# Optimization experiments

Measured on AMD Instinct MI355X. Metric: run time of the kernel, lower is better.

Reference implementation:

```python
import jax, jax.numpy as jnp
import numpy as np

EPS_DIST = 1e-7  # matches torch: log((d+1)/(d+1e-7))


def _cdist(x, p):
    # x: (B, N, D), p: (P, D) -> (B, N, P) Euclidean distances
    x2 = jnp.sum(x * x, axis=-1, keepdims=True)        # (B, N, 1)
    p2 = jnp.sum(p * p, axis=-1)                       # (P,)
    d2 = x2 + p2[None, None, :] - 2.0 * jnp.einsum('bnd,pd->bnp', x, p)
    return jnp.sqrt(jnp.maximum(d2, 1e-12))


def setup_inputs() -> dict:
    key = jax.random.key(0)
    k1, k2, k3 = jax.random.split(key, 3)
    B, C, H, W = 32, 2048, 14, 14
    num_classes, npc = 200, 10
    P = num_classes * npc
    x = jax.random.normal(k1, (B, C, H, W), dtype=jnp.float32)
    prototypes = jax.random.normal(k2, (1, P, C), dtype=jnp.float32)
    fc_w = jax.random.normal(k3, (num_classes, P), dtype=jnp.float32) * 0.02
    return {"x": x, "prototypes": prototypes, "fc_w": fc_w}


def reference(x, prototypes, fc_w):
    B, C, H, W = x.shape
    feats = x.reshape(B, C, H * W).transpose(0, 2, 1)   # (B, HW, D)
    protos = prototypes[0]                              # (P, D)
    num_classes = fc_w.shape[0]
    npc = protos.shape[0] // num_classes

    distances = _cdist(feats, protos)                   # (B, HW, P)
    similarity = jnp.log((distances + 1.0) / (distances + EPS_DIST))
    max_similarity = jnp.max(similarity, axis=1)        # (B, P)
    min_distances = jnp.min(distances, axis=1)          # (B, P)
    min_distances_per_class = min_distances.reshape(B, num_classes, npc)
    scores = max_similarity @ fc_w.T                    # (B, num_classes)
    return scores, min_distances_per_class
```

## Files before the change

### kernel.cpp

```cpp
#include <hip/hip_runtime.h>

#define INF_BITS 0x7F800000u
#define AS1 __attribute__((address_space(1)))
#define AS3 __attribute__((address_space(3)))

typedef float f32x4 __attribute__((ext_vector_type(4)));
typedef int i32x4 __attribute__((ext_vector_type(4)));
typedef int i32x8 __attribute__((ext_vector_type(8)));
typedef unsigned int u32x2 __attribute__((ext_vector_type(2)));
typedef unsigned int u32x4 __attribute__((ext_vector_type(4)));

template <int SEL>
static __device__ __forceinline__ float dq8(unsigned int w) {
  return __builtin_amdgcn_cvt_f32_fp8((int)w, SEL);
}

__global__ __launch_bounds__(256) void k_prep_p(const float* __restrict__ protos,
                                                unsigned char* __restrict__ pTf,
                                                float* __restrict__ p2,
                                                unsigned int* __restrict__ outu) {
  const int row = blockIdx.x;
  const int tid = threadIdx.x;
  const int gi = row * 256 + tid;
  if (gi < 64000) outu[6400 + gi] = INF_BITS;
  __shared__ float red[4];
  float s = 0.f;
  unsigned int w0 = 0u, w1 = 0u;
  if (row < 2000) {
    const float* src = protos + (size_t)row * 2048 + tid * 8;
    f32x4 a = *(const f32x4*)src;
    f32x4 c = *(const f32x4*)(src + 4);
    w0 = (unsigned int)__builtin_amdgcn_cvt_pk_fp8_f32(a.x, a.y, 0, false);
    w0 = (unsigned int)__builtin_amdgcn_cvt_pk_fp8_f32(a.z, a.w, (int)w0, true);
    w1 = (unsigned int)__builtin_amdgcn_cvt_pk_fp8_f32(c.x, c.y, 0, false);
    w1 = (unsigned int)__builtin_amdgcn_cvt_pk_fp8_f32(c.z, c.w, (int)w1, true);
    float q;
    q = dq8<0>(w0); s += q * q;
    q = dq8<1>(w0); s += q * q;
    q = dq8<2>(w0); s += q * q;
    q = dq8<3>(w0); s += q * q;
    q = dq8<0>(w1); s += q * q;
    q = dq8<1>(w1); s += q * q;
    q = dq8<2>(w1); s += q * q;
    q = dq8<3>(w1); s += q * q;
  }
  *(u32x2*)(pTf + (size_t)row * 2048 + tid * 8) = (u32x2){w0, w1};
  #pragma unroll
  for (int off = 32; off; off >>= 1) s += __shfl_xor(s, off);
  if ((tid & 63) == 0) red[tid >> 6] = s;
  __syncthreads();
  if (tid == 0) p2[row] = red[0] + red[1] + red[2] + red[3];
}

__global__ __launch_bounds__(256) void k_prep_x(const float* __restrict__ x,
                                                unsigned char* __restrict__ xTf,
                                                float* __restrict__ x2p,
                                                float* __restrict__ x2) {
  const int kt = blockIdx.x;
  const int b  = blockIdx.y;
  const int tid = threadIdx.x;
  if (b == 32) {
    u32x4* pad = (u32x4*)(xTf + (size_t)6272 * 2048);
    #pragma unroll
    for (int j = tid; j < 512; j += 256)
      pad[kt * 512 + j] = (u32x4){0u, 0u, 0u, 0u};
    if (kt == 0 && tid < 128) x2[6272 + tid] = __uint_as_float(INF_BITS);
    return;
  }
  __shared__ unsigned char Ls[64][208];
  const float* src = x + ((size_t)b * 2048 + (size_t)kt * 64) * 196;
  for (int idx = tid; idx < 3136; idx += 256) {
    const int kk = idx / 49, c4 = idx - kk * 49;
    f32x4 v = *(const f32x4*)(src + (size_t)kk * 196 + c4 * 4);
    unsigned int w = (unsigned int)__builtin_amdgcn_cvt_pk_fp8_f32(v.x, v.y, 0, false);
    w = (unsigned int)__builtin_amdgcn_cvt_pk_fp8_f32(v.z, v.w, (int)w, true);
    *(unsigned int*)&Ls[kk][c4 * 4] = w;
  }
  __syncthreads();
  if (tid < 196) {
    float s = 0.f;
    #pragma unroll
    for (int j = 0; j < 64; ++j) {
      float v = dq8<0>((unsigned int)Ls[j][tid]);
      s += v * v;
    }
    x2p[kt * 6272 + b * 196 + tid] = s;
  }
  unsigned char* dstb = xTf + (size_t)b * 196 * 2048 + kt * 64;
  for (int idx = tid; idx < 784; idx += 256) {
    const int n = idx >> 2, q = idx & 3;
    const int k0 = q * 16;
    u32x4 v;
    #pragma unroll
    for (int j = 0; j < 4; ++j) {
      v[j] = (unsigned int)Ls[k0 + 4 * j + 0][n] |
             ((unsigned int)Ls[k0 + 4 * j + 1][n] << 8) |
             ((unsigned int)Ls[k0 + 4 * j + 2][n] << 16) |
             ((unsigned int)Ls[k0 + 4 * j + 3][n] << 24);
    }
    *(u32x4*)(dstb + (size_t)n * 2048 + k0) = v;
  }
}

__global__ void k_x2r(const float* __restrict__ x2p, float* __restrict__ x2) {
  int i = blockIdx.x * blockDim.x + threadIdx.x;
  if (i >= 6272) return;
  float s = 0.f;
  #pragma unroll
  for (int c = 0; c < 32; ++c) s += x2p[c * 6272 + i];
  x2[i] = s;
}

__global__ __launch_bounds__(512, 2) void k_main(
    const unsigned char* __restrict__ pTf, const unsigned char* __restrict__ xTf,
    const float* __restrict__ p2, const float* __restrict__ x2,
    unsigned int* __restrict__ outu) {
  const int orig = blockIdx.x;
  const int wgid = (orig & 7) * 25 + (orig >> 3);
  const int ptpair = wgid / 50;
  const int rem = wgid - ptpair * 50;
  const int ptile = ptpair * 2 + (rem & 1);
  const int mtile = rem >> 1;
  const int p0 = ptile * 256;
  const int m0 = mtile * 256;
  const int tid = threadIdx.x;
  const int lane = tid & 63;
  const int w = tid >> 6;
  const int wp = w >> 2;
  const int wn = w & 3;
  const int lr = lane & 15;
  const int lg = lane >> 4;

  __shared__ __align__(16) char S[131072];

  f32x4 acc[8][4];
  #pragma unroll
  for (int mi = 0; mi < 8; ++mi)
    #pragma unroll
    for (int ni = 0; ni < 4; ++ni)
      acc[mi][ni] = (f32x4){0.f, 0.f, 0.f, 0.f};

  const int rowbase = tid >> 3;
  const int chunk = (tid & 7) ^ (rowbase & 7);
  const char* gA = (const char*)pTf + (size_t)(p0 + rowbase) * 2048 + chunk * 16;
  const char* gB = (const char*)xTf + (size_t)(m0 + rowbase) * 2048 + chunk * 16;
  const int wbase = w * 1024;

#define STAGE_A(c_, kt_, h_) do {                                              \
    const char* s_ = gA + (size_t)((h_) * 128 * 2048) + (size_t)(kt_) * 128;   \
    _Pragma("unroll")                                                          \
    for (int j_ = 0; j_ < 2; ++j_)                                             \
      __builtin_amdgcn_global_load_lds(                                        \
          (const AS1 void*)(s_ + (size_t)j_ * 64 * 2048),                      \
          (AS3 void*)(S + (c_) * 32768 + (h_) * 16384 + j_ * 8192 + wbase),    \
          16, 0, 0);                                                           \
  } while (0)
#define STAGE_B(c_, kt_, h_) do {                                              \
    const char* s_ = gB + (size_t)((h_) * 128 * 2048) + (size_t)(kt_) * 128;   \
    _Pragma("unroll")                                                          \
    for (int j_ = 0; j_ < 2; ++j_)                                             \
      __builtin_amdgcn_global_load_lds(                                        \
          (const AS1 void*)(s_ + (size_t)j_ * 64 * 2048),                      \
          (AS3 void*)(S + 65536 + (c_) * 32768 + (h_) * 16384 + j_ * 8192 + wbase), \
          16, 0, 0);                                                           \
  } while (0)

  const int swz = ((lr & 7) << 4);
  const int koffA = (lg * 32) ^ swz;
  const int arow = (wp * 128 + lr) * 128;
  const int brow = (wn * 64 + lr) * 128;

#define READ_A4(dst_, c_, hf_)                                                 \
    _Pragma("unroll")                                                          \
    for (int mi_ = 0; mi_ < 4; ++mi_) {                                        \
      const char* p_ = S + (c_) * 32768 + arow + ((hf_) * 4 + mi_) * 2048;     \
      u32x4 lo_ = *(const u32x4*)(p_ + koffA);                                 \
      u32x4 hi_ = *(const u32x4*)(p_ + (koffA ^ 16));                          \
      dst_[mi_] = __builtin_bit_cast(i32x8,                                    \
          __builtin_shufflevector(lo_, hi_, 0, 1, 2, 3, 4, 5, 6, 7));          \
    }
#define READ_B4(dst_, c_)                                                      \
    _Pragma("unroll")                                                          \
    for (int ni_ = 0; ni_ < 4; ++ni_) {                                        \
      const char* p_ = S + 65536 + (c_) * 32768 + brow + ni_ * 2048;           \
      u32x4 lo_ = *(const u32x4*)(p_ + koffA);                                 \
      u32x4 hi_ = *(const u32x4*)(p_ + (koffA ^ 16));                          \
      dst_[ni_] = __builtin_bit_cast(i32x8,                                    \
          __builtin_shufflevector(lo_, hi_, 0, 1, 2, 3, 4, 5, 6, 7));          \
    }

#define PH_BAR() do { __builtin_amdgcn_sched_barrier(0);                       \
    __builtin_amdgcn_s_barrier(); __builtin_amdgcn_sched_barrier(0); } while (0)
#define LGKM0() do { asm volatile("s_waitcnt lgkmcnt(0)" ::: "memory");        \
    __builtin_amdgcn_sched_barrier(0); } while (0)
#define MFMA_Q(mlo_, af_, bf_) do { __builtin_amdgcn_s_setprio(1);             \
    _Pragma("unroll")                                                          \
    for (int mi_ = 0; mi_ < 4; ++mi_)                                          \
      _Pragma("unroll")                                                        \
      for (int ni_ = 0; ni_ < 4; ++ni_)                                        \
        acc[(mlo_) + mi_][ni_] =                                               \
            __builtin_amdgcn_mfma_scale_f32_16x16x128_f8f6f4(                  \
                af_[mi_], bf_[ni_], acc[(mlo_) + mi_][ni_],                    \
                0, 0, 0, 0x7F7F7F7F, 0, 0x7F7F7F7F);                           \
    __builtin_amdgcn_s_setprio(0); } while (0)

#define KT_BODY(kt_, c_, sa_, sb_, vm_) do {                                   \
    i32x8 af[4], bf[4];                                                        \
    READ_B4(bf, c_);                                                           \
    READ_A4(af, c_, 0);                                                        \
    if (sa_) { STAGE_A((c_) ^ 1, (kt_) + 1, 0); STAGE_A((c_) ^ 1, (kt_) + 1, 1); } \
    PH_BAR(); LGKM0();                                                         \
    MFMA_Q(0, af, bf);                                                         \
    PH_BAR();                                                                  \
    READ_A4(af, c_, 1);                                                        \
    if (sb_) { STAGE_B(c_, (kt_) + 2, 0); STAGE_B(c_, (kt_) + 2, 1); }         \
    PH_BAR(); LGKM0();                                                         \
    MFMA_Q(4, af, bf);                                                         \
    if ((vm_) == 4)      asm volatile("s_waitcnt vmcnt(4)" ::: "memory");      \
    else if ((vm_) == 0) asm volatile("s_waitcnt vmcnt(0)" ::: "memory");      \
    __builtin_amdgcn_sched_barrier(0);                                         \
    PH_BAR();                                                                  \
  } while (0)

  STAGE_A(0, 0, 0); STAGE_A(0, 0, 1);
  STAGE_B(0, 0, 0); STAGE_B(0, 0, 1);
  STAGE_B(1, 1, 0); STAGE_B(1, 1, 1);
  asm volatile("s_waitcnt vmcnt(4)" ::: "memory");
  __builtin_amdgcn_sched_barrier(0);
  __builtin_amdgcn_s_barrier();
  __builtin_amdgcn_sched_barrier(0);

  #pragma unroll 1
  for (int it = 0; it < 7; ++it) {
    KT_BODY(2 * it, 0, 1, 1, 4);
    KT_BODY(2 * it + 1, 1, 1, 1, 4);
  }
  KT_BODY(14, 0, 1, 0, 0);
  KT_BODY(15, 1, 0, 0, -1);
#undef KT_BODY
#undef MFMA_Q
#undef READ_A4
#undef READ_B4
#undef STAGE_A
#undef STAGE_B

  const int wm_base = m0 + wn * 64;
  const int b_lo = wm_base / 196;
  int b_hi = (wm_base + 63) / 196;
  if (b_hi > 31) b_hi = 31;
  const bool wave_ok = (b_lo < 32);
  float x2v[4];
  int seg0[4];
  #pragma unroll
  for (int ni = 0; ni < 4; ++ni) {
    const int m = wm_base + ni * 16 + lr;
    x2v[ni] = x2[m];
    seg0[ni] = ((m / 196) == b_lo);
  }
  const float INF = __uint_as_float(INF_BITS);
  #pragma unroll
  for (int mi = 0; mi < 8; ++mi) {
    const int prow = p0 + wp * 128 + mi * 16 + 4 * lg;
    #pragma unroll
    for (int j = 0; j < 4; ++j) {
      const int p = prow + j;
      const float pp = p2[p];
      float ma = INF, mb = INF;
      #pragma unroll
      for (int ni = 0; ni < 4; ++ni) {
        const float d2 = x2v[ni] + pp - 2.f * acc[mi][ni][j];
        ma = fminf(ma, seg0[ni] ? d2 : INF);
        mb = fminf(mb, seg0[ni] ? INF : d2);
      }
      #pragma unroll
      for (int off = 1; off < 16; off <<= 1) {
        ma = fminf(ma, __shfl_xor(ma, off));
        mb = fminf(mb, __shfl_xor(mb, off));
      }
      if (lr == 0 && p < 2000 && wave_ok) {
        atomicMin(&outu[6400 + b_lo * 2000 + p], __float_as_uint(fmaxf(ma, 0.f)));
        if (b_hi != b_lo)
          atomicMin(&outu[6400 + b_hi * 2000 + p], __float_as_uint(fmaxf(mb, 0.f)));
      }
    }
  }
}

__global__ void k_post(float* __restrict__ out, float* __restrict__ simbuf) {
  int i = blockIdx.x * blockDim.x + threadIdx.x;
  if (i >= 64000) return;
  float d2 = out[6400 + i];
  float d = sqrtf(fmaxf(d2, 1e-12f));
  out[6400 + i] = d;
  simbuf[i] = logf((d + 1.0f) / (d + 1e-7f));
}

__global__ __launch_bounds__(256) void k_scores(const float* __restrict__ fc_w,
                                                const float* __restrict__ simbuf,
                                                float* __restrict__ out) {
  const int id = blockIdx.x * 4 + (threadIdx.x >> 6);
  const int lane = threadIdx.x & 63;
  const int b = id / 200;
  const int c = id - b * 200;
  const f32x4* sv = (const f32x4*)(simbuf + (size_t)b * 2000);
  const f32x4* wv = (const f32x4*)(fc_w + (size_t)c * 2000);
  float s = 0.f;
  #pragma unroll
  for (int it = 0; it < 8; ++it) {
    int i = lane + it * 64;
    if (i < 500) {
      f32x4 a = sv[i], w4 = wv[i];
      s += a.x * w4.x + a.y * w4.y + a.z * w4.z + a.w * w4.w;
    }
  }
  #pragma unroll
  for (int off = 32; off; off >>= 1) s += __shfl_xor(s, off);
  if (lane == 0) out[b * 200 + c] = s;
}

extern "C" void kernel_launch(void* const* d_in, const int* in_sizes, int n_in,
                              void* d_out, int out_size, void* d_ws, size_t ws_size,
                              hipStream_t stream) {
  const float* x      = (const float*)d_in[0];
  const float* protos = (const float*)d_in[1];
  const float* fc_w   = (const float*)d_in[2];
  float* out = (float*)d_out;

  char* wsb = (char*)d_ws;
  unsigned char* pTf = (unsigned char*)wsb;
  unsigned char* xTf = (unsigned char*)(wsb + 4194304);
  float* p2   = (float*)(wsb + 17301504);
  float* x2   = (float*)(wsb + 17309696);
  float* x2p  = (float*)(wsb + 17335296);
  float* simb = (float*)(wsb + 17335296);

  k_prep_p<<<2048, 256, 0, stream>>>(protos, pTf, p2, (unsigned int*)d_out);
  k_prep_x<<<dim3(32, 33), 256, 0, stream>>>(x, xTf, x2p, x2);
  k_x2r<<<25, 256, 0, stream>>>(x2p, x2);
  k_main<<<200, 512, 0, stream>>>(pTf, xTf, p2, x2, (unsigned int*)d_out);
  k_post<<<250, 256, 0, stream>>>(out, simb);
  k_scores<<<1600, 256, 0, stream>>>(fc_w, simb, out);
}
```

Baseline: 87.52 us.

## Interleave per-row A fragment LDS reads with MFMAs and cut barriers per k-step

The inner k-step no longer reads four A fragments, waits, runs sixteen MFMAs and repeats. It now streams one A row fragment at a time, double-buffered in two registers, so each LDS read overlaps the MFMAs of the previous row. The A prefetch is issued at the top of the step, and the B prefetch and vmcnt wait move after all MFMAs, leaving two barriers per step instead of four. This should hide LDS latency and reduce synchronisation stalls, but it relies on the compiler leaving the reads and MFMAs in that order and on the LDS buffer reuse staying race-free. The final step skips the trailing barriers.

```diff
diff --git a/kernel.cpp b/kernel.cpp
--- a/kernel.cpp
+++ b/kernel.cpp
@@ -170,15 +170,13 @@
   const int arow = (wp * 128 + lr) * 128;
   const int brow = (wn * 64 + lr) * 128;
 
-#define READ_A4(dst_, c_, hf_)                                                 \
-    _Pragma("unroll")                                                          \
-    for (int mi_ = 0; mi_ < 4; ++mi_) {                                        \
-      const char* p_ = S + (c_) * 32768 + arow + ((hf_) * 4 + mi_) * 2048;     \
-      u32x4 lo_ = *(const u32x4*)(p_ + koffA);                                 \
-      u32x4 hi_ = *(const u32x4*)(p_ + (koffA ^ 16));                          \
-      dst_[mi_] = __builtin_bit_cast(i32x8,                                    \
-          __builtin_shufflevector(lo_, hi_, 0, 1, 2, 3, 4, 5, 6, 7));          \
-    }
+#define READ_A1(dst_, c_, a_) do {                                             \
+    const char* p_ = S + (c_) * 32768 + arow + (a_) * 2048;                    \
+    u32x4 lo_ = *(const u32x4*)(p_ + koffA);                                   \
+    u32x4 hi_ = *(const u32x4*)(p_ + (koffA ^ 16));                            \
+    dst_ = __builtin_bit_cast(i32x8,                                           \
+        __builtin_shufflevector(lo_, hi_, 0, 1, 2, 3, 4, 5, 6, 7));            \
+  } while (0)
 #define READ_B4(dst_, c_)                                                      \
     _Pragma("unroll")                                                          \
     for (int ni_ = 0; ni_ < 4; ++ni_) {                                        \
@@ -189,57 +187,58 @@
           __builtin_shufflevector(lo_, hi_, 0, 1, 2, 3, 4, 5, 6, 7));          \
     }
 
-#define PH_BAR() do { __builtin_amdgcn_sched_barrier(0);                       \
-    __builtin_amdgcn_s_barrier(); __builtin_amdgcn_sched_barrier(0); } while (0)
-#define LGKM0() do { asm volatile("s_waitcnt lgkmcnt(0)" ::: "memory");        \
-    __builtin_amdgcn_sched_barrier(0); } while (0)
-#define MFMA_Q(mlo_, af_, bf_) do { __builtin_amdgcn_s_setprio(1);             \
+#define SCHED() __builtin_amdgcn_sched_barrier(0)
+#define SBAR() do { SCHED(); __builtin_amdgcn_s_barrier(); SCHED(); } while (0)
+#define LGKM0() do { asm volatile("s_waitcnt lgkmcnt(0)" ::: "memory"); SCHED(); } while (0)
+#define MFMA4(mi_, af_, bf_) do { __builtin_amdgcn_s_setprio(1);               \
     _Pragma("unroll")                                                          \
-    for (int mi_ = 0; mi_ < 4; ++mi_)                                          \
-      _Pragma("unroll")                                                        \
-      for (int ni_ = 0; ni_ < 4; ++ni_)                                        \
-        acc[(mlo_) + mi_][ni_] =                                               \
-            __builtin_amdgcn_mfma_scale_f32_16x16x128_f8f6f4(                  \
-                af_[mi_], bf_[ni_], acc[(mlo_) + mi_][ni_],                    \
-                0, 0, 0, 0x7F7F7F7F, 0, 0x7F7F7F7F);                           \
+    for (int ni_ = 0; ni_ < 4; ++ni_)                                          \
+      acc[mi_][ni_] = __builtin_amdgcn_mfma_scale_f32_16x16x128_f8f6f4(        \
+          af_, bf_[ni_], acc[mi_][ni_], 0, 0, 0, 0x7F7F7F7F, 0, 0x7F7F7F7F);   \
     __builtin_amdgcn_s_setprio(0); } while (0)
 
-#define KT_BODY(kt_, c_, sa_, sb_, vm_) do {                                   \
-    i32x8 af[4], bf[4];                                                        \
+#define KT_BODY(kt_, c_, sa_, sb_, vm_, tail_) do {                            \
+    if (sa_) { STAGE_A((c_) ^ 1, (kt_) + 1, 0); STAGE_A((c_) ^ 1, (kt_) + 1, 1); } \
+    i32x8 bf[4], af0, af1;                                                     \
     READ_B4(bf, c_);                                                           \
-    READ_A4(af, c_, 0);                                                        \
-    if (sa_) { STAGE_A((c_) ^ 1, (kt_) + 1, 0); STAGE_A((c_) ^ 1, (kt_) + 1, 1); } \
-    PH_BAR(); LGKM0();                                                         \
-    MFMA_Q(0, af, bf);                                                         \
-    PH_BAR();                                                                  \
-    READ_A4(af, c_, 1);                                                        \
-    if (sb_) { STAGE_B(c_, (kt_) + 2, 0); STAGE_B(c_, (kt_) + 2, 1); }         \
-    PH_BAR(); LGKM0();                                                         \
-    MFMA_Q(4, af, bf);                                                         \
-    if ((vm_) == 4)      asm volatile("s_waitcnt vmcnt(4)" ::: "memory");      \
-    else if ((vm_) == 0) asm volatile("s_waitcnt vmcnt(0)" ::: "memory");      \
-    __builtin_amdgcn_sched_barrier(0);                                         \
-    PH_BAR();                                                                  \
+    READ_A1(af0, c_, 0);                                                       \
+    READ_A1(af1, c_, 1); MFMA4(0, af0, bf); SCHED();                           \
+    READ_A1(af0, c_, 2); MFMA4(1, af1, bf); SCHED();                           \
+    READ_A1(af1, c_, 3); MFMA4(2, af0, bf); SCHED();                           \
+    READ_A1(af0, c_, 4); MFMA4(3, af1, bf); SCHED();                           \
+    READ_A1(af1, c_, 5); MFMA4(4, af0, bf); SCHED();                           \
+    READ_A1(af0, c_, 6); MFMA4(5, af1, bf); SCHED();                           \
+    READ_A1(af1, c_, 7); MFMA4(6, af0, bf); SCHED();                           \
+    MFMA4(7, af1, bf);                                                         \
+    if (!(tail_)) {                                                            \
+      LGKM0();                                                                 \
+      SBAR();                                               \
+      if (sb_) { STAGE_B(c_, (kt_) + 2, 0); STAGE_B(c_, (kt_) + 2, 1); }       \
+      if ((vm_) == 4)      asm volatile("s_waitcnt vmcnt(4)" ::: "memory");    \
+      else if ((vm_) == 0) asm volatile("s_waitcnt vmcnt(0)" ::: "memory");    \
+      SCHED();                                                                 \
+      SBAR();                                             \
+    }                                                                          \
   } while (0)
 
   STAGE_A(0, 0, 0); STAGE_A(0, 0, 1);
   STAGE_B(0, 0, 0); STAGE_B(0, 0, 1);
   STAGE_B(1, 1, 0); STAGE_B(1, 1, 1);
   asm volatile("s_waitcnt vmcnt(4)" ::: "memory");
-  __builtin_amdgcn_sched_barrier(0);
+  SCHED();
   __builtin_amdgcn_s_barrier();
-  __builtin_amdgcn_sched_barrier(0);
+  SCHED();
 
   #pragma unroll 1
   for (int it = 0; it < 7; ++it) {
-    KT_BODY(2 * it, 0, 1, 1, 4);
-    KT_BODY(2 * it + 1, 1, 1, 1, 4);
-  }
-  KT_BODY(14, 0, 1, 0, 0);
-  KT_BODY(15, 1, 0, 0, -1);
+    KT_BODY(2 * it, 0, 1, 1, 4, 0);
+    KT_BODY(2 * it + 1, 1, 1, 1, 4, 0);
+  }
+  KT_BODY(14, 0, 1, 0, 0, 0);
+  KT_BODY(15, 1, 0, 0, -1, 1);
 #undef KT_BODY
-#undef MFMA_Q
-#undef READ_A4
+#undef MFMA4
+#undef READ_A1
 #undef READ_B4
 #undef STAGE_A
 #undef STAGE_B
```

Measured after the change: 83.56 us. 1.05x faster.
